# Optimization experiments

Hardware: AMD Instinct MI355X
Metric: run time of the kernel (lower is better)

The kernel has to match this reference:

```python
import jax, jax.numpy as jnp
import numpy as np

B, T, C, H = 4, 2048, 1024, 16
D = C // H
SCALE = D ** -0.5


def setup_inputs() -> dict:
    key = jax.random.key(0)
    ks = jax.random.split(key, 5)
    x = jax.random.normal(ks[0], (B, T, C), dtype=jnp.float32)
    key_padding_mask = jnp.zeros((B, T), dtype=bool)  # True = masked key
    W_qkv = jax.random.normal(ks[1], (C, 3 * C), dtype=jnp.float32) * (C ** -0.5)
    b_qkv = jax.random.normal(ks[2], (3 * C,), dtype=jnp.float32) * 0.02
    W_proj = jax.random.normal(ks[3], (C, C), dtype=jnp.float32) * (C ** -0.5)
    b_proj = jax.random.normal(ks[4], (C,), dtype=jnp.float32) * 0.02
    return {"x": x, "key_padding_mask": key_padding_mask, "W_qkv": W_qkv,
            "b_qkv": b_qkv, "W_proj": W_proj, "b_proj": b_proj}


def reference(x, key_padding_mask, W_qkv, b_qkv, W_proj, b_proj):
    Bx, Tx, Cx = x.shape
    qkv = x @ W_qkv + b_qkv                      # [B,T,3C]
    qkv = qkv.reshape(Bx, Tx, 3, H, D)
    q = jnp.transpose(qkv[:, :, 0], (0, 2, 1, 3))  # [B,H,T,D]
    k = jnp.transpose(qkv[:, :, 1], (0, 2, 1, 3))
    v = jnp.transpose(qkv[:, :, 2], (0, 2, 1, 3))
    attn = jnp.einsum('bhqd,bhkd->bhqk', q, k) * SCALE  # [B,H,T,T]
    causal = jnp.triu(jnp.ones((Tx, Tx), dtype=bool), k=1)  # True = masked
    neg_inf = jnp.finfo(attn.dtype).min
    attn = jnp.where(causal[None, None, :, :], neg_inf, attn)
    attn = jnp.where(key_padding_mask[:, None, None, :], neg_inf, attn)
    attn = jax.nn.softmax(attn, axis=-1)
    out = jnp.einsum('bhqk,bhkd->bhqd', attn, v)  # [B,H,T,D]
    out = jnp.transpose(out, (0, 2, 1, 3)).reshape(Bx, Tx, Cx)
    return out @ W_proj + b_proj
```

## Files before the change

kernel.cpp:

```cpp
#include <hip/hip_runtime.h>


typedef __bf16 bf16;
typedef __bf16 bf16x4 __attribute__((ext_vector_type(4)));
typedef __bf16 bf16x8 __attribute__((ext_vector_type(8)));
typedef float f32x4 __attribute__((ext_vector_type(4)));

#define MFMA(a, b, c) __builtin_amdgcn_mfma_f32_16x16x32_bf16((a), (b), (c), 0, 0, 0)

typedef const __attribute__((address_space(1))) void* gas_ptr;
typedef __attribute__((address_space(3))) void* las_ptr;

__device__ __forceinline__ void gload_lds16(const bf16* g, bf16* lds) {
  __builtin_amdgcn_global_load_lds((gas_ptr)g, (las_ptr)lds, 16, 0, 0);
}

__global__ __launch_bounds__(256) void k_cvt(const float* __restrict__ src,
                                             bf16* __restrict__ dst, int n4) {
  int i = blockIdx.x * 256 + threadIdx.x;
  if (i >= n4) return;
  float4 v = ((const float4*)src)[i];
  bf16x4 o = { (bf16)v.x, (bf16)v.y, (bf16)v.z, (bf16)v.w };
  ((bf16x4*)dst)[i] = o;
}

__global__ __launch_bounds__(256) void k_transpose(const float* __restrict__ src,
                                                   bf16* __restrict__ dst,
                                                   int R, int C) {
  __shared__ float tile[32][33];
  int c0 = blockIdx.x * 32, r0 = blockIdx.y * 32;
  int x = threadIdx.x & 31, y = threadIdx.x >> 5;
#pragma unroll
  for (int i = 0; i < 4; ++i)
    tile[y + i * 8][x] = src[(size_t)(r0 + y + i * 8) * C + (c0 + x)];
  __syncthreads();
#pragma unroll
  for (int i = 0; i < 4; ++i)
    dst[(size_t)(c0 + y + i * 8) * R + (r0 + x)] = (bf16)tile[x][y + i * 8];
}

__global__ void k_maskflags(const unsigned char* __restrict__ kpm,
                            int* __restrict__ flags) {
  int i = threadIdx.x;
  const uint4* p = (const uint4*)(kpm + i * 128);
  unsigned acc = 0;
#pragma unroll
  for (int j = 0; j < 8; ++j) { uint4 v = p[j]; acc |= v.x | v.y | v.z | v.w; }
  flags[i] = (acc != 0) ? 1 : 0;
}

template <int EPI>
__global__ __launch_bounds__(256, 3)
void k_gemm_bt(const bf16* __restrict__ A, const bf16* __restrict__ Bt,
               const float* __restrict__ bias, float* __restrict__ fout,
               bf16* __restrict__ qp, bf16* __restrict__ kp,
               bf16* __restrict__ vtp, int M, int N, int K) {
  __shared__ bf16 Ab[2][128 * 32];
  __shared__ bf16 Bb[2][128 * 32];
  const int tid = threadIdx.x;
  const int wave = tid >> 6, lane = tid & 63;
  const int m0 = blockIdx.x * 128, n0 = blockIdx.y * 128;
  const int wr = wave >> 1, wc = wave & 1;
  const int lrow = lane & 15, kb = (lane >> 4) * 8;
  f32x4 acc[4][4] = {};
  const int nkt = K >> 5;

  auto stage = [&](int buf, int kt) {
#pragma unroll
    for (int i = 0; i < 2; ++i) {
      int c = i * 4 + wave;
      const bf16* ga = A + (size_t)(m0 + c * 16 + (lane >> 2)) * K + kt * 32 + (lane & 3) * 8;
      gload_lds16(ga, &Ab[buf][c * 512]);
      const bf16* gb = Bt + (size_t)(n0 + c * 16 + (lane >> 2)) * K + kt * 32 + (lane & 3) * 8;
      gload_lds16(gb, &Bb[buf][c * 512]);
    }
  };

  stage(0, 0);
  asm volatile("s_waitcnt vmcnt(0)" ::: "memory");
  __syncthreads();
  int cur = 0;
  for (int kt = 0; kt < nkt; ++kt) {
    if (kt + 1 < nkt) stage(cur ^ 1, kt + 1);
    bf16x8 af[4], bfr[4];
#pragma unroll
    for (int m = 0; m < 4; ++m)
      af[m] = *(const bf16x8*)&Ab[cur][(wr * 64 + m * 16 + lrow) * 32 + kb];
#pragma unroll
    for (int n = 0; n < 4; ++n)
      bfr[n] = *(const bf16x8*)&Bb[cur][(wc * 64 + n * 16 + lrow) * 32 + kb];
#pragma unroll
    for (int m = 0; m < 4; ++m)
#pragma unroll
      for (int n = 0; n < 4; ++n)
        acc[m][n] = MFMA(af[m], bfr[n], acc[m][n]);
    asm volatile("s_waitcnt vmcnt(0)" ::: "memory");
    __syncthreads();
    cur ^= 1;
  }

#pragma unroll
  for (int m = 0; m < 4; ++m) {
#pragma unroll
    for (int n = 0; n < 4; ++n) {
      const int col = n0 + wc * 64 + n * 16 + lrow;
      const int row0 = m0 + wr * 64 + m * 16 + (lane >> 4) * 4;
      const float bv = bias[col];
      if (EPI == 0) {
        const int which = col >> 10;
        const int h = (col >> 6) & 15, d = col & 63;
        const int b = row0 >> 11, t0 = row0 & 2047;
        const int bh = b * 16 + h;
        if (which == 2) {
          bf16x4 pk;
#pragma unroll
          for (int j = 0; j < 4; ++j) pk[j] = (bf16)(acc[m][n][j] + bv);
          *(bf16x4*)&vtp[((size_t)bh * 64 + d) * 2048 + t0] = pk;
        } else {
          bf16* dstp = (which == 0) ? qp : kp;
          const float sc = (which == 0) ? 0.18033688011112042f : 1.0f;
#pragma unroll
          for (int j = 0; j < 4; ++j)
            dstp[((size_t)bh * 2048 + (t0 + j)) * 64 + d] = (bf16)((acc[m][n][j] + bv) * sc);
        }
      } else {
#pragma unroll
        for (int j = 0; j < 4; ++j)
          fout[(size_t)(row0 + j) * N + col] = acc[m][n][j] + bv;
      }
    }
  }
}

__global__ __launch_bounds__(256, 3)
void k_flash(const bf16* __restrict__ Q, const bf16* __restrict__ Kg,
             const bf16* __restrict__ Vt, const unsigned char* __restrict__ kpm,
             const int* __restrict__ tflags, bf16* __restrict__ O) {
  const int bh = blockIdx.x;
  const int b = bh >> 4, h = bh & 15;
  const int qt = 15 - (int)blockIdx.y;
  const int tid = threadIdx.x, wave = tid >> 6, lane = tid & 63;
  const int lrow = lane & 15, g = lane >> 4;

  __shared__ bf16 Kt[16 * 512];
  __shared__ bf16 Vts[16 * 512];
  __shared__ bf16 PT[4][2048];

  const bf16* Kbh = Kg + (size_t)bh * 2048 * 64;
  const bf16* Vbh = Vt + (size_t)bh * 64 * 2048;

  const int ptb2 = g * 256 + lrow * 8;

  const bf16* Qbase = Q + ((size_t)bh * 2048 + qt * 128 + wave * 32) * 64;
  bf16x8 qf[2][2];
#pragma unroll
  for (int m = 0; m < 2; ++m)
#pragma unroll
    for (int ks = 0; ks < 2; ++ks)
      qf[m][ks] = *(const bf16x8*)&Qbase[(m * 16 + lrow) * 64 + ks * 32 + g * 8];

  const bf16 one_bf = (bf16)1.0f;
  const bf16x8 ones8 = { one_bf, one_bf, one_bf, one_bf, one_bf, one_bf, one_bf, one_bf };

  f32x4 oacc[2][4] = {};
  f32x4 osum[2] = {};

  for (int kvt = 0; kvt <= qt; ++kvt) {
#pragma unroll
    for (int i = 0; i < 4; ++i) {
      int c = i * 4 + wave;
      gload_lds16(Kbh + (size_t)(kvt * 128 + (c >> 1) * 16 + lrow) * 64 + (c & 1) * 32 + g * 8,
                  &Kt[c * 512]);
    }
#pragma unroll
    for (int i = 0; i < 4; ++i) {
      int c = i * 4 + wave;
      gload_lds16(Vbh + (size_t)((c & 3) * 16 + lrow) * 2048 + kvt * 128 + (c >> 2) * 32 + g * 8,
                  &Vts[c * 512]);
    }
    asm volatile("s_waitcnt vmcnt(0)" ::: "memory");
    __builtin_amdgcn_s_barrier();
    __builtin_amdgcn_sched_barrier(0);

    const bool diag = (kvt == qt);
    const int nmax = diag ? (2 * wave + 2) : 8;
    const int ksmax = diag ? (wave + 1) : 4;

    f32x4 s[2][8];
    __builtin_amdgcn_s_setprio(1);
#pragma unroll
    for (int n = 0; n < 8; ++n) {
      if (n < nmax) {
        bf16x8 kf0 = *(const bf16x8*)&Kt[(n * 2 + 0) * 512 + lane * 8];
        bf16x8 kf1 = *(const bf16x8*)&Kt[(n * 2 + 1) * 512 + lane * 8];
#pragma unroll
        for (int m = 0; m < 2; ++m) {
          f32x4 t = {};
          t = MFMA(qf[m][0], kf0, t);
          t = MFMA(qf[m][1], kf1, t);
          s[m][n] = t;
        }
      }
    }
    __builtin_amdgcn_s_setprio(0);

    if (tflags[b * 16 + kvt]) {
#pragma unroll
      for (int n = 0; n < 8; ++n) {
        if (n < nmax) {
          const int col = kvt * 128 + n * 16 + lrow;
          if (kpm[b * 2048 + col]) {
#pragma unroll
            for (int m = 0; m < 2; ++m)
#pragma unroll
              for (int j = 0; j < 4; ++j) s[m][n][j] = -1e30f;
          }
        }
      }
    }
    if (diag) {
#pragma unroll
      for (int n = 0; n < 8; ++n) {
        if (n < nmax) {
          const int ccol = n * 16 + lrow;
#pragma unroll
          for (int m = 0; m < 2; ++m)
#pragma unroll
            for (int j = 0; j < 4; ++j) {
              const int crow = wave * 32 + m * 16 + g * 4 + j;
              if (ccol > crow) s[m][n][j] = -1e30f;
            }
        }
      }
    }

#pragma unroll
    for (int m = 0; m < 2; ++m) {
#pragma unroll
      for (int n = 0; n < 8; ++n) {
        if (n < nmax) {
          bf16x4 pk;
#pragma unroll
          for (int j = 0; j < 4; ++j) pk[j] = (bf16)exp2f(s[m][n][j]);
          const int woff = (n * 16 + lrow) * 32 + g * 8;
          *(bf16x4*)((char*)&PT[wave][0] + woff) = pk;
        }
      }
      asm volatile("s_waitcnt lgkmcnt(0)" ::: "memory");
      __builtin_amdgcn_sched_barrier(0);
#pragma unroll
      for (int ks = 0; ks < 4; ++ks) {
        if (ks < ksmax) {
          bf16x4 plo, phi;
          las_ptr pa_ = (las_ptr)((char*)&PT[wave][0] + ptb2);
          asm volatile("ds_read_b64_tr_b16 %0, %1 offset:%2"
                       : "=v"(plo) : "v"(pa_), "i"(ks * 1024));
          asm volatile("ds_read_b64_tr_b16 %0, %1 offset:%2"
                       : "=v"(phi) : "v"(pa_), "i"(ks * 1024 + 128));
          bf16x8 vf[4];
#pragma unroll
          for (int nt = 0; nt < 4; ++nt)
            vf[nt] = *(const bf16x8*)&Vts[(ks * 4 + nt) * 512 + lane * 8];
          asm volatile("s_waitcnt lgkmcnt(0)" ::: "memory");
          __builtin_amdgcn_sched_barrier(0);
          bf16x8 pa = __builtin_shufflevector(plo, phi, 0, 1, 2, 3, 4, 5, 6, 7);
          __builtin_amdgcn_s_setprio(1);
#pragma unroll
          for (int nt = 0; nt < 4; ++nt)
            oacc[m][nt] = MFMA(pa, vf[nt], oacc[m][nt]);
          osum[m] = MFMA(pa, ones8, osum[m]);
          __builtin_amdgcn_s_setprio(0);
        }
      }
    }

    __builtin_amdgcn_s_barrier();
    __builtin_amdgcn_sched_barrier(0);
  }

#pragma unroll
  for (int m = 0; m < 2; ++m)
#pragma unroll
    for (int nt = 0; nt < 4; ++nt)
#pragma unroll
      for (int j = 0; j < 4; ++j) {
        const int t = qt * 128 + wave * 32 + m * 16 + g * 4 + j;
        const int c = h * 64 + nt * 16 + lrow;
        O[((size_t)b * 2048 + t) * 1024 + c] = (bf16)(oacc[m][nt][j] / osum[m][j]);
      }
}

extern "C" void kernel_launch(void* const* d_in, const int* in_sizes, int n_in,
                              void* d_out, int out_size, void* d_ws, size_t ws_size,
                              hipStream_t stream) {
  const float* x = (const float*)d_in[0];
  const unsigned char* kpm = (const unsigned char*)d_in[1];
  const float* Wqkv = (const float*)d_in[2];
  const float* bqkv = (const float*)d_in[3];
  const float* Wproj = (const float*)d_in[4];
  const float* bproj = (const float*)d_in[5];
  float* out = (float*)d_out;
  char* ws = (char*)d_ws;

  bf16* xb     = (bf16*)(ws + 0);
  bf16* WqkvT  = (bf16*)(ws + 16777216);
  bf16* WprojT = (bf16*)(ws + 23068672);
  bf16* Qb     = (bf16*)(ws + 25165824);
  bf16* Kb     = (bf16*)(ws + 41943040);
  bf16* Vtb    = (bf16*)(ws + 58720256);
  bf16* AOb    = (bf16*)(ws + 75497472);
  int*  tflags = (int*)(ws + 0);

  k_cvt<<<8192, 256, 0, stream>>>(x, xb, 2097152);
  k_transpose<<<dim3(96, 32), 256, 0, stream>>>(Wqkv, WqkvT, 1024, 3072);
  k_transpose<<<dim3(32, 32), 256, 0, stream>>>(Wproj, WprojT, 1024, 1024);
  k_gemm_bt<0><<<dim3(64, 24), 256, 0, stream>>>(xb, WqkvT, bqkv, nullptr, Qb, Kb,
                                                 Vtb, 8192, 3072, 1024);
  k_maskflags<<<1, 64, 0, stream>>>(kpm, tflags);
  k_flash<<<dim3(64, 16), 256, 0, stream>>>(Qb, Kb, Vtb, kpm, tflags, AOb);
  k_gemm_bt<1><<<dim3(64, 8), 256, 0, stream>>>(AOb, WprojT, bproj, out, nullptr,
                                                nullptr, nullptr, 8192, 1024, 1024);
}
```

Baseline: 187.4 us.

## Rework GEMM to 256x128 tiles, 512 threads, K=64 steps with MFMA-ordered LDS layout

```diff
diff --git a/kernel.cpp b/kernel.cpp
--- a/kernel.cpp
+++ b/kernel.cpp
@@ -50,52 +50,69 @@
 }
 
 template <int EPI>
-__global__ __launch_bounds__(256, 3)
-void k_gemm_bt(const bf16* __restrict__ A, const bf16* __restrict__ Bt,
-               const float* __restrict__ bias, float* __restrict__ fout,
-               bf16* __restrict__ qp, bf16* __restrict__ kp,
-               bf16* __restrict__ vtp, int M, int N, int K) {
-  __shared__ bf16 Ab[2][128 * 32];
-  __shared__ bf16 Bb[2][128 * 32];
+__global__ __launch_bounds__(512, 2)
+void k_gemm2(const bf16* __restrict__ A, const bf16* __restrict__ Bt,
+             const float* __restrict__ bias, float* __restrict__ fout,
+             bf16* __restrict__ qp, bf16* __restrict__ kp,
+             bf16* __restrict__ vtp, int M, int N, int K) {
+  __shared__ bf16 Ab[2][32 * 512];
+  __shared__ bf16 Bb[2][16 * 512];
   const int tid = threadIdx.x;
   const int wave = tid >> 6, lane = tid & 63;
-  const int m0 = blockIdx.x * 128, n0 = blockIdx.y * 128;
+  const int lrow = lane & 15, g = lane >> 4;
+  const int m0 = blockIdx.x * 256, n0 = blockIdx.y * 128;
   const int wr = wave >> 1, wc = wave & 1;
-  const int lrow = lane & 15, kb = (lane >> 4) * 8;
   f32x4 acc[4][4] = {};
-  const int nkt = K >> 5;
+  const int nkt = K >> 6;
 
   auto stage = [&](int buf, int kt) {
 #pragma unroll
+    for (int i = 0; i < 4; ++i) {
+      int c = i * 8 + wave;
+      gload_lds16(A + (size_t)(m0 + (c >> 1) * 16 + lrow) * K + kt * 64 + (c & 1) * 32 + g * 8,
+                  &Ab[buf][c * 512]);
+    }
+#pragma unroll
     for (int i = 0; i < 2; ++i) {
-      int c = i * 4 + wave;
-      const bf16* ga = A + (size_t)(m0 + c * 16 + (lane >> 2)) * K + kt * 32 + (lane & 3) * 8;
-      gload_lds16(ga, &Ab[buf][c * 512]);
-      const bf16* gb = Bt + (size_t)(n0 + c * 16 + (lane >> 2)) * K + kt * 32 + (lane & 3) * 8;
-      gload_lds16(gb, &Bb[buf][c * 512]);
+      int c = i * 8 + wave;
+      gload_lds16(Bt + (size_t)(n0 + (c >> 1) * 16 + lrow) * K + kt * 64 + (c & 1) * 32 + g * 8,
+                  &Bb[buf][c * 512]);
     }
   };
 
   stage(0, 0);
-  asm volatile("s_waitcnt vmcnt(0)" ::: "memory");
-  __syncthreads();
   int cur = 0;
   for (int kt = 0; kt < nkt; ++kt) {
-    if (kt + 1 < nkt) stage(cur ^ 1, kt + 1);
-    bf16x8 af[4], bfr[4];
-#pragma unroll
-    for (int m = 0; m < 4; ++m)
-      af[m] = *(const bf16x8*)&Ab[cur][(wr * 64 + m * 16 + lrow) * 32 + kb];
-#pragma unroll
-    for (int n = 0; n < 4; ++n)
-      bfr[n] = *(const bf16x8*)&Bb[cur][(wc * 64 + n * 16 + lrow) * 32 + kb];
-#pragma unroll
-    for (int m = 0; m < 4; ++m)
+    const bool pref = (kt + 1 < nkt);
+    if (pref) {
+      stage(cur ^ 1, kt + 1);
+      asm volatile("s_waitcnt vmcnt(6)" ::: "memory");
+    } else {
+      asm volatile("s_waitcnt vmcnt(0)" ::: "memory");
+    }
+    __builtin_amdgcn_s_barrier();
+    __builtin_amdgcn_sched_barrier(0);
+
+#pragma unroll
+    for (int ks = 0; ks < 2; ++ks) {
+      bf16x8 af[4], bfr[4];
+#pragma unroll
+      for (int m = 0; m < 4; ++m)
+        af[m] = *(const bf16x8*)&Ab[cur][((wr * 4 + m) * 2 + ks) * 512 + lane * 8];
 #pragma unroll
       for (int n = 0; n < 4; ++n)
-        acc[m][n] = MFMA(af[m], bfr[n], acc[m][n]);
-    asm volatile("s_waitcnt vmcnt(0)" ::: "memory");
-    __syncthreads();
+        bfr[n] = *(const bf16x8*)&Bb[cur][((wc * 4 + n) * 2 + ks) * 512 + lane * 8];
+      __builtin_amdgcn_s_setprio(1);
+#pragma unroll
+      for (int m = 0; m < 4; ++m)
+#pragma unroll
+        for (int n = 0; n < 4; ++n)
+          acc[m][n] = MFMA(af[m], bfr[n], acc[m][n]);
+      __builtin_amdgcn_s_setprio(0);
+    }
+
+    __builtin_amdgcn_s_barrier();
+    __builtin_amdgcn_sched_barrier(0);
     cur ^= 1;
   }
 
@@ -104,7 +121,7 @@
 #pragma unroll
     for (int n = 0; n < 4; ++n) {
       const int col = n0 + wc * 64 + n * 16 + lrow;
-      const int row0 = m0 + wr * 64 + m * 16 + (lane >> 4) * 4;
+      const int row0 = m0 + wr * 64 + m * 16 + g * 4;
       const float bv = bias[col];
       if (EPI == 0) {
         const int which = col >> 10;
@@ -314,10 +331,10 @@
   k_cvt<<<8192, 256, 0, stream>>>(x, xb, 2097152);
   k_transpose<<<dim3(96, 32), 256, 0, stream>>>(Wqkv, WqkvT, 1024, 3072);
   k_transpose<<<dim3(32, 32), 256, 0, stream>>>(Wproj, WprojT, 1024, 1024);
-  k_gemm_bt<0><<<dim3(64, 24), 256, 0, stream>>>(xb, WqkvT, bqkv, nullptr, Qb, Kb,
-                                                 Vtb, 8192, 3072, 1024);
+  k_gemm2<0><<<dim3(32, 24), 512, 0, stream>>>(xb, WqkvT, bqkv, nullptr, Qb, Kb,
+                                               Vtb, 8192, 3072, 1024);
   k_maskflags<<<1, 64, 0, stream>>>(kpm, tflags);
   k_flash<<<dim3(64, 16), 256, 0, stream>>>(Qb, Kb, Vtb, kpm, tflags, AOb);
-  k_gemm_bt<1><<<dim3(64, 8), 256, 0, stream>>>(AOb, WprojT, bproj, out, nullptr,
-                                                nullptr, nullptr, 8192, 1024, 1024);
-}
+  k_gemm2<1><<<dim3(32, 8), 512, 0, stream>>>(AOb, WprojT, bproj, out, nullptr,
+                                              nullptr, nullptr, 8192, 1024, 1024);
+}
```

After: 239.1 us. 27.6% more time.
